# Optimization experiments

Hardware: AMD Instinct MI355X
Metric: run time of the kernel (lower is better)

Reference implementation:

```python
import jax, jax.numpy as jnp
import numpy as np
from jax import lax

# quantization constants (from init_kwargs)
IN_SCALE = 0.05
IN_ZP = 128
W_SCALE = 0.02
W_ZP = 128
OUT_SCALE = 0.1
OUT_ZP = 0
PADDING = 1


def setup_inputs() -> dict:
    key = jax.random.key(0)
    k1, k2, k3 = jax.random.split(key, 3)
    x_float = jax.random.normal(k1, (8, 32, 512, 512), dtype=jnp.float32)
    weight = jax.random.randint(k2, (32, 32, 3, 3), 0, 256, dtype=jnp.int32)  # uint8-like
    bias = jax.random.randint(k3, (32,), 0, 100, dtype=jnp.int32)  # int32 accumulator bias
    return {"x_float": x_float, "weight": weight, "bias": bias}


def reference(x_float, weight, bias):
    # quantize input to uint8 range, then recenter
    x_q = jnp.round(x_float / IN_SCALE) + IN_ZP
    x_q = jnp.clip(x_q, 0, 255).astype(jnp.int32) - IN_ZP
    # recenter weights
    w_q = weight - W_ZP
    # integer conv emulated in float (NCHW, OIHW), 'same' padding=1
    y_int = lax.conv_general_dilated(
        x_q.astype(jnp.float32), w_q.astype(jnp.float32),
        window_strides=(1, 1), padding=[(PADDING, PADDING), (PADDING, PADDING)],
        dimension_numbers=("NCHW", "OIHW", "NCHW"),
    ).astype(jnp.int32)
    y_int = y_int + bias[None, :, None, None]
    # requantize + dequantize + relu (fused elementwise)
    scale_float = IN_SCALE * W_SCALE / OUT_SCALE
    y_q = jnp.clip(jnp.round(y_int.astype(jnp.float32) * scale_float), -127, 127).astype(jnp.int32)
    y = (y_q - OUT_ZP).astype(jnp.float32) * OUT_SCALE
    return jax.nn.relu(y)
```

## Files before the change

kernel.cpp:

```cpp
#include <hip/hip_runtime.h>


#define N_IMG 8
#define CIN   32
#define COUT  32
#define HD    512
#define WD    512
#define TH    8
#define TW    64
#define XROWS 10
#define XCOLS 68
#define NTASK (2 * XROWS * XCOLS)

typedef int intx4 __attribute__((ext_vector_type(4)));

__global__ __launch_bounds__(256, 4) void conv8_fused(const float* __restrict__ x,
                                                      const int* __restrict__ wq,
                                                      const int* __restrict__ bias,
                                                      float* __restrict__ out)
{
    __shared__ alignas(16) unsigned char xs[XROWS * XCOLS * CIN];
    __shared__ alignas(16) char wp[6 * 32 * 64];

    const int tid = threadIdx.x;
    const int bx = blockIdx.x;
    const int by = blockIdx.y;
    const int n  = blockIdx.z;

#pragma unroll
    for (int k = 0; k < 12; ++k) {
        const int d    = tid + k * 256;
        const int row  = d >> 4;
        const int k0   = (d & 15) * 4;
        const int khp  = row >> 5;
        const int cout = row & 31;
        const int kh   = khp >> 1;
        const int pr   = khp & 1;
        const int sel  = k0 >> 5;
        const int kw   = pr * 2 + sel;
        unsigned int pk = 0u;
        if (kw < 3) {
            const int cin0 = k0 & 31;
            const int* wqp = wq + ((cout * CIN + cin0) * 3 + kh) * 3 + kw;
            unsigned int b0 = (unsigned int)(wqp[0]  - 128) & 0xffu;
            unsigned int b1 = (unsigned int)(wqp[9]  - 128) & 0xffu;
            unsigned int b2 = (unsigned int)(wqp[18] - 128) & 0xffu;
            unsigned int b3 = (unsigned int)(wqp[27] - 128) & 0xffu;
            pk = b0 | (b1 << 8) | (b2 << 16) | (b3 << 24);
        }
        *(unsigned int*)(wp + d * 4) = pk;
    }

    const int h0  = by * TH - 1;
    const int wt0 = bx * TW - 1;

    float bufA[16], bufB[16];

    auto issue = [&](int k, float (&buf)[16]) {
        const int idx = tid + k * 256;
        if (idx >= NTASK) return;
        const int half = (idx >= XROWS * XCOLS) ? 1 : 0;
        const int rem  = idx - half * (XROWS * XCOLS);
        const int row  = rem / XCOLS;
        const int pc   = rem - row * XCOLS;
        const int h = h0 + row, w = wt0 + pc;
        if ((unsigned)h < (unsigned)HD && (unsigned)w < (unsigned)WD) {
            const float* xp = x + ((size_t)(n * CIN + half * 16) * HD + h) * WD + w;
#pragma unroll
            for (int c = 0; c < 16; ++c)
                buf[c] = xp[(size_t)c * (HD * WD)];
        }
    };
    auto flush = [&](int k, float (&buf)[16]) {
        const int idx = tid + k * 256;
        if (idx >= NTASK) return;
        const int half = (idx >= XROWS * XCOLS) ? 1 : 0;
        const int rem  = idx - half * (XROWS * XCOLS);
        const int row  = rem / XCOLS;
        const int pc   = rem - row * XCOLS;
        const int h = h0 + row, w = wt0 + pc;
        const bool inb = (unsigned)h < (unsigned)HD && (unsigned)w < (unsigned)WD;
        unsigned int pk[4] = {0u, 0u, 0u, 0u};
        if (inb) {
#pragma unroll
            for (int c4 = 0; c4 < 4; ++c4) {
                unsigned int b[4];
#pragma unroll
                for (int j = 0; j < 4; ++j) {
                    float q = rintf(buf[c4 * 4 + j] / 0.05f);
                    q = fminf(fmaxf(q, -128.0f), 127.0f);
                    b[j] = (unsigned int)(int)q & 0xffu;
                }
                pk[c4] = b[0] | (b[1] << 8) | (b[2] << 16) | (b[3] << 24);
            }
        }
        *(uint4*)(xs + (size_t)(row * XCOLS + pc) * CIN + half * 16) =
            make_uint4(pk[0], pk[1], pk[2], pk[3]);
    };

    issue(0, bufA);
    issue(1, bufB); flush(0, bufA);
    issue(2, bufA); flush(1, bufB);
    issue(3, bufB); flush(2, bufA);
    issue(4, bufA); flush(3, bufB);
    issue(5, bufB); flush(4, bufA);
    flush(5, bufB);

    __syncthreads();

    const int lane = tid & 63;
    const int wave = tid >> 6;
    const int l15  = lane & 15;
    const int quad = lane >> 4;

    intx4 Af[3][2][2];
#pragma unroll
    for (int kh = 0; kh < 3; ++kh)
#pragma unroll
        for (int p = 0; p < 2; ++p)
#pragma unroll
            for (int hf = 0; hf < 2; ++hf)
                Af[kh][p][hf] = *(const intx4*)(wp + (((kh * 2 + p) * 32 + hf * 16 + l15) << 6) + quad * 16);

    int bi0[4], bi1[4];
#pragma unroll
    for (int r = 0; r < 4; ++r) { bi0[r] = bias[quad * 4 + r]; bi1[r] = bias[16 + quad * 4 + r]; }

    const int wseg = wave * 16;
    const unsigned char* bbase = xs + (size_t)(wseg + l15) * CIN + quad * 16;

#pragma unroll
    for (int it = 0; it < 4; ++it) {
        intx4 Bw[4][2];
#pragma unroll
        for (int r = 0; r < 4; ++r)
#pragma unroll
            for (int p = 0; p < 2; ++p)
                Bw[r][p] = *(const intx4*)(bbase + (size_t)((2 * it + r) * XCOLS) * CIN + p * 64);

        intx4 acc[2][2];
#pragma unroll
        for (int o = 0; o < 2; ++o)
#pragma unroll
            for (int hf = 0; hf < 2; ++hf)
                acc[o][hf] = (intx4){0, 0, 0, 0};

#pragma unroll
        for (int o = 0; o < 2; ++o)
#pragma unroll
            for (int kh = 0; kh < 3; ++kh)
#pragma unroll
                for (int p = 0; p < 2; ++p) {
                    const intx4 b = Bw[o + kh][p];
                    acc[o][0] = __builtin_amdgcn_mfma_i32_16x16x64_i8(Af[kh][p][0], b, acc[o][0], 0, 0, 0);
                    acc[o][1] = __builtin_amdgcn_mfma_i32_16x16x64_i8(Af[kh][p][1], b, acc[o][1], 0, 0, 0);
                }

#pragma unroll
        for (int o = 0; o < 2; ++o) {
            const int h = by * TH + 2 * it + o;
            float* op0 = out + (((size_t)n * COUT + quad * 4) * HD + h) * WD + bx * TW + wseg + l15;
            float* op1 = op0 + (size_t)16 * HD * WD;
#pragma unroll
            for (int r = 0; r < 4; ++r) {
                int v0 = acc[o][0][r] + bi0[r];
                float yq0 = rintf((float)v0 * 0.01f);
                yq0 = fminf(fmaxf(yq0, -127.f), 127.f);
                op0[(size_t)r * (HD * WD)] = fmaxf(yq0 * 0.1f, 0.f);
                int v1 = acc[o][1][r] + bi1[r];
                float yq1 = rintf((float)v1 * 0.01f);
                yq1 = fminf(fmaxf(yq1, -127.f), 127.f);
                op1[(size_t)r * (HD * WD)] = fmaxf(yq1 * 0.1f, 0.f);
            }
        }
    }
}

extern "C" void kernel_launch(void* const* d_in, const int* in_sizes, int n_in,
                              void* d_out, int out_size, void* d_ws, size_t ws_size,
                              hipStream_t stream) {
    const float* x  = (const float*)d_in[0];
    const int*   wq = (const int*)d_in[1];
    const int*   bi = (const int*)d_in[2];
    float* out = (float*)d_out;
    (void)d_ws; (void)ws_size;

    conv8_fused<<<dim3(WD / TW, HD / TH, N_IMG), dim3(256), 0, stream>>>(x, wq, bi, out);
}
```

Before: 495.9 us.

## Vectorize input tile loads with float4 and split LDS into per-half channel planes

Input staging now loads four consecutive pixels per thread with 16-byte float4 global loads for the 64 interior columns, and handles the two halo columns in a separate scalar path. The LDS tile is reorganized into two planes of 16 channels each, and the MFMA B-operand addressing is updated to match the new layout. The aim is fewer, wider global load instructions in the memory-bound quantize-and-stage phase. In exchange each thread holds 64 floats live, which raises register pressure, and the explicit double-buffered issue/flush pipelining is replaced by a sched_barrier.

```diff
diff --git a/kernel.cpp b/kernel.cpp
--- a/kernel.cpp
+++ b/kernel.cpp
@@ -10,16 +10,17 @@
 #define TW    64
 #define XROWS 10
 #define XCOLS 68
-#define NTASK (2 * XROWS * XCOLS)
+#define PLANE (XROWS * XCOLS * 16)
 
 typedef int intx4 __attribute__((ext_vector_type(4)));
+typedef float floatx4 __attribute__((ext_vector_type(4)));
 
 __global__ __launch_bounds__(256, 4) void conv8_fused(const float* __restrict__ x,
                                                       const int* __restrict__ wq,
                                                       const int* __restrict__ bias,
                                                       float* __restrict__ out)
 {
-    __shared__ alignas(16) unsigned char xs[XROWS * XCOLS * CIN];
+    __shared__ alignas(16) unsigned char xs[2 * PLANE];
     __shared__ alignas(16) char wp[6 * 32 * 64];
 
     const int tid = threadIdx.x;
@@ -51,60 +52,75 @@
         *(unsigned int*)(wp + d * 4) = pk;
     }
 
-    const int h0  = by * TH - 1;
-    const int wt0 = bx * TW - 1;
-
-    float bufA[16], bufB[16];
-
-    auto issue = [&](int k, float (&buf)[16]) {
-        const int idx = tid + k * 256;
-        if (idx >= NTASK) return;
-        const int half = (idx >= XROWS * XCOLS) ? 1 : 0;
-        const int rem  = idx - half * (XROWS * XCOLS);
-        const int row  = rem / XCOLS;
-        const int pc   = rem - row * XCOLS;
-        const int h = h0 + row, w = wt0 + pc;
-        if ((unsigned)h < (unsigned)HD && (unsigned)w < (unsigned)WD) {
-            const float* xp = x + ((size_t)(n * CIN + half * 16) * HD + h) * WD + w;
-#pragma unroll
-            for (int c = 0; c < 16; ++c)
-                buf[c] = xp[(size_t)c * (HD * WD)];
+    const int h0 = by * TH - 1;
+    for (int t = tid; t < 360; t += 256) {
+        if (t < 320) {
+            const int g    = t & 15;
+            const int half = (t >> 4) & 1;
+            const int row  = t >> 5;
+            const int h    = h0 + row;
+            const bool inb = (unsigned)h < (unsigned)HD;
+            floatx4 v[16];
+            if (inb) {
+                const float* xp = x + ((size_t)(n * CIN + half * 16) * HD + h) * WD + bx * TW + g * 4;
+#pragma unroll
+                for (int c = 0; c < 16; ++c)
+                    v[c] = *(const floatx4*)(xp + (size_t)c * (HD * WD));
+            }
+            __builtin_amdgcn_sched_barrier(0);
+            unsigned char* dst = xs + half * PLANE + ((size_t)row * XCOLS + 1 + g * 4) * 16;
+#pragma unroll
+            for (int j = 0; j < 4; ++j) {
+                unsigned int pk[4] = {0u, 0u, 0u, 0u};
+                if (inb) {
+#pragma unroll
+                    for (int c4 = 0; c4 < 4; ++c4) {
+                        unsigned int bb = 0u;
+#pragma unroll
+                        for (int cc = 0; cc < 4; ++cc) {
+                            float q = rintf(v[c4 * 4 + cc][j] / 0.05f);
+                            q = fminf(fmaxf(q, -128.0f), 127.0f);
+                            bb |= ((unsigned int)(int)q & 0xffu) << (cc * 8);
+                        }
+                        pk[c4] = bb;
+                    }
+                }
+                *(uint4*)(dst + j * 16) = make_uint4(pk[0], pk[1], pk[2], pk[3]);
+            }
+        } else {
+            const int u    = t - 320;
+            const int pc   = (u & 1) ? 65 : 0;
+            const int half = (u >> 1) & 1;
+            const int row  = u >> 2;
+            const int h    = h0 + row;
+            const int w    = bx * TW - 1 + pc;
+            const bool inb = (unsigned)h < (unsigned)HD && (unsigned)w < (unsigned)WD;
+            float v[16];
+            if (inb) {
+                const float* xp = x + ((size_t)(n * CIN + half * 16) * HD + h) * WD + w;
+#pragma unroll
+                for (int c = 0; c < 16; ++c)
+                    v[c] = xp[(size_t)c * (HD * WD)];
+            }
+            __builtin_amdgcn_sched_barrier(0);
+            unsigned int pk[4] = {0u, 0u, 0u, 0u};
+            if (inb) {
+#pragma unroll
+                for (int c4 = 0; c4 < 4; ++c4) {
+                    unsigned int bb = 0u;
+#pragma unroll
+                    for (int cc = 0; cc < 4; ++cc) {
+                        float q = rintf(v[c4 * 4 + cc] / 0.05f);
+                        q = fminf(fmaxf(q, -128.0f), 127.0f);
+                        bb |= ((unsigned int)(int)q & 0xffu) << (cc * 8);
+                    }
+                    pk[c4] = bb;
+                }
+            }
+            *(uint4*)(xs + half * PLANE + ((size_t)row * XCOLS + pc) * 16) =
+                make_uint4(pk[0], pk[1], pk[2], pk[3]);
         }
-    };
-    auto flush = [&](int k, float (&buf)[16]) {
-        const int idx = tid + k * 256;
-        if (idx >= NTASK) return;
-        const int half = (idx >= XROWS * XCOLS) ? 1 : 0;
-        const int rem  = idx - half * (XROWS * XCOLS);
-        const int row  = rem / XCOLS;
-        const int pc   = rem - row * XCOLS;
-        const int h = h0 + row, w = wt0 + pc;
-        const bool inb = (unsigned)h < (unsigned)HD && (unsigned)w < (unsigned)WD;
-        unsigned int pk[4] = {0u, 0u, 0u, 0u};
-        if (inb) {
-#pragma unroll
-            for (int c4 = 0; c4 < 4; ++c4) {
-                unsigned int b[4];
-#pragma unroll
-                for (int j = 0; j < 4; ++j) {
-                    float q = rintf(buf[c4 * 4 + j] / 0.05f);
-                    q = fminf(fmaxf(q, -128.0f), 127.0f);
-                    b[j] = (unsigned int)(int)q & 0xffu;
-                }
-                pk[c4] = b[0] | (b[1] << 8) | (b[2] << 16) | (b[3] << 24);
-            }
-        }
-        *(uint4*)(xs + (size_t)(row * XCOLS + pc) * CIN + half * 16) =
-            make_uint4(pk[0], pk[1], pk[2], pk[3]);
-    };
-
-    issue(0, bufA);
-    issue(1, bufB); flush(0, bufA);
-    issue(2, bufA); flush(1, bufB);
-    issue(3, bufB); flush(2, bufA);
-    issue(4, bufA); flush(3, bufB);
-    issue(5, bufB); flush(4, bufA);
-    flush(5, bufB);
+    }
 
     __syncthreads();
 
@@ -127,7 +143,8 @@
     for (int r = 0; r < 4; ++r) { bi0[r] = bias[quad * 4 + r]; bi1[r] = bias[16 + quad * 4 + r]; }
 
     const int wseg = wave * 16;
-    const unsigned char* bbase = xs + (size_t)(wseg + l15) * CIN + quad * 16;
+    const unsigned char* bbase = xs + (size_t)(quad & 1) * PLANE
+                               + ((size_t)(wseg + l15 + (quad >> 1))) * 16;
 
 #pragma unroll
     for (int it = 0; it < 4; ++it) {
@@ -136,7 +153,7 @@
         for (int r = 0; r < 4; ++r)
 #pragma unroll
             for (int p = 0; p < 2; ++p)
-                Bw[r][p] = *(const intx4*)(bbase + (size_t)((2 * it + r) * XCOLS) * CIN + p * 64);
+                Bw[r][p] = *(const intx4*)(bbase + (size_t)((2 * it + r) * XCOLS + 2 * p) * 16);
 
         intx4 acc[2][2];
 #pragma unroll
```

New measurement: 484.0 us. 1.02x faster.
